# Kernel tuning notes

Hardware: AMD Instinct MI355X
Metric: run time of the kernel (lower is better)

Reference implementation:

```python
import jax, jax.numpy as jnp
import numpy as np

EPS = 1e-5


def _bn(v, gamma, beta, mean, var):
    # v: [n, c, L, 1]; per-channel eval-mode batchnorm
    scale = gamma / jnp.sqrt(var + EPS)
    return v * scale[None, :, None, None] + (beta - mean * scale)[None, :, None, None]


def _conv1x1(v, w, b):
    # v: [n, c, L, 1], w: [o, c], b: [o] -> [n, o, L, 1]
    y = jnp.einsum('ncl,oc->nol', v[..., 0], w) + b[None, :, None]
    return y[..., None]


def setup_inputs() -> dict:
    key = jax.random.key(0)
    ks = jax.random.split(key, 16)
    N, C, H, W, MIP = 8, 256, 112, 112, 8
    return {
        'x': jax.random.normal(ks[0], (N, C, H, W), dtype=jnp.float32),
        'bn1_gamma': jax.random.uniform(ks[1], (C,), dtype=jnp.float32),
        'bn1_beta': jax.random.normal(ks[2], (C,), dtype=jnp.float32) * 0.1,
        'bn1_mean': jax.random.normal(ks[3], (C,), dtype=jnp.float32) * 0.1,
        'bn1_var': jax.random.uniform(ks[4], (C,), dtype=jnp.float32) + 0.5,
        'bn2_gamma': jax.random.uniform(ks[5], (C,), dtype=jnp.float32),
        'bn2_beta': jax.random.normal(ks[6], (C,), dtype=jnp.float32) * 0.1,
        'bn2_mean': jax.random.normal(ks[7], (C,), dtype=jnp.float32) * 0.1,
        'bn2_var': jax.random.uniform(ks[8], (C,), dtype=jnp.float32) + 0.5,
        'ds_w': jax.random.normal(ks[9], (MIP, C), dtype=jnp.float32) * (1.0 / np.sqrt(C)),
        'ds_b': jax.random.normal(ks[10], (MIP,), dtype=jnp.float32) * 0.01,
        'us_w': jax.random.normal(ks[11], (C, MIP), dtype=jnp.float32) * (1.0 / np.sqrt(MIP)),
        'us_b': jax.random.normal(ks[12], (C,), dtype=jnp.float32) * 0.01,
    }


def reference(x, bn1_gamma, bn1_beta, bn1_mean, bn1_var,
              bn2_gamma, bn2_beta, bn2_mean, bn2_var,
              ds_w, ds_b, us_w, us_b):
    identity = x
    # dual-axis average pooling
    x_h = jnp.mean(x, axis=3, keepdims=True)                 # [n, c, h, 1]
    x_w = jnp.mean(x, axis=2, keepdims=True).transpose(0, 1, 3, 2)  # [n, c, w, 1]
    # batchnorm (eval mode)
    x_h = _bn(x_h, bn1_gamma, bn1_beta, bn1_mean, bn1_var)
    x_w = _bn(x_w, bn2_gamma, bn2_beta, bn2_mean, bn2_var)
    # channel-reduce 1x1 conv + relu
    d_h = jax.nn.relu(_conv1x1(x_h, ds_w, ds_b))             # [n, mip, h, 1]
    d_w = jax.nn.relu(_conv1x1(x_w, ds_w, ds_b))             # [n, mip, w, 1]
    # channel-expand 1x1 conv + sigmoid
    a_h = jax.nn.sigmoid(_conv1x1(d_h, us_w, us_b))          # [n, c, h, 1]
    a_w = jax.nn.sigmoid(_conv1x1(d_w, us_w, us_b))          # [n, c, w, 1]
    a_w = a_w.transpose(0, 1, 3, 2)                          # [n, c, 1, w]
    out = identity * a_w * a_h + identity
    # h_swish: x * relu6(x + 3) / 6
    return out * jnp.clip(out + 3.0, 0.0, 6.0) * (1.0 / 6.0)
```

## Files before the change

kernel.cpp:

```cpp
#include <hip/hip_runtime.h>
#include <math.h>

#define NN 8
#define CC 256
#define HH 112
#define WW 112
#define MIP 8
#define EPS 1e-5f

typedef float nvec4 __attribute__((ext_vector_type(4)));


__global__ __launch_bounds__(256) void pool_kernel(const float* __restrict__ x,
                                                   float* __restrict__ pool) {
    __shared__ float rowpart[HH][29];
    __shared__ float4 colpart[8][28];
    const int b = blockIdx.x;
    const int n = b / CC;
    const int c = b % CC;
    const int t = threadIdx.x;

    const nvec4* p4 = (const nvec4*)(x + (size_t)b * (HH * WW));

    if (t < 224) {
        const int g = t / 28;
        const int j = t % 28;
        float4 ca = make_float4(0.f, 0.f, 0.f, 0.f);
#pragma unroll
        for (int k = 0; k < 14; ++k) {
            const int r = g + 8 * k;
            nvec4 v = __builtin_nontemporal_load(&p4[r * 28 + j]);
            ca.x += v.x; ca.y += v.y; ca.z += v.z; ca.w += v.w;
            rowpart[r][j] = v.x + v.y + v.z + v.w;
        }
        colpart[g][j] = ca;
    }
    __syncthreads();

    if (t < HH) {
        float s = 0.f;
#pragma unroll
        for (int j = 0; j < 28; ++j) s += rowpart[t][j];
        pool[((size_t)(n * HH + t)) * CC + c] = s * (1.0f / WW);
    } else if (t < 112 + WW) {
        const int w = t - 112;
        const float* cp = (const float*)&colpart[0][0];
        float s = 0.f;
#pragma unroll
        for (int g = 0; g < 8; ++g) s += cp[g * 112 + w];
        pool[(size_t)(NN * HH * CC) + ((size_t)(n * WW + w)) * CC + c] = s * (1.0f / HH);
    }
}

__global__ __launch_bounds__(256) void att_kernel(
    float* __restrict__ pool,
    const float* __restrict__ bn1_g, const float* __restrict__ bn1_b,
    const float* __restrict__ bn1_m, const float* __restrict__ bn1_v,
    const float* __restrict__ bn2_g, const float* __restrict__ bn2_b,
    const float* __restrict__ bn2_m, const float* __restrict__ bn2_v,
    const float* __restrict__ ds_w, const float* __restrict__ ds_b,
    const float* __restrict__ us_w, const float* __restrict__ us_b) {
    __shared__ float s[CC];
    __shared__ float dsh[MIP];

    const int branch = blockIdx.y;
    const int c = threadIdx.x;

    const float* g  = branch ? bn2_g : bn1_g;
    const float* be = branch ? bn2_b : bn1_b;
    const float* mn = branch ? bn2_m : bn1_m;
    const float* vr = branch ? bn2_v : bn1_v;

    const size_t idx = (size_t)branch * (NN * HH * CC) + (size_t)blockIdx.x * CC + c;

    float v = pool[idx];
    float scale = g[c] * rsqrtf(vr[c] + EPS);
    float vb = v * scale + (be[c] - mn[c] * scale);
    s[c] = vb;
    __syncthreads();

    {
        const int grp = c >> 5;
        const int l = c & 31;
        float partial = 0.f;
#pragma unroll
        for (int k = 0; k < CC / 32; ++k) {
            const int cc = l + k * 32;
            partial += ds_w[grp * CC + cc] * s[cc];
        }
#pragma unroll
        for (int off = 16; off > 0; off >>= 1)
            partial += __shfl_down(partial, off, 32);
        if (l == 0) dsh[grp] = fmaxf(partial + ds_b[grp], 0.f);
    }
    __syncthreads();

    float acc = us_b[c];
#pragma unroll
    for (int m = 0; m < MIP; ++m) acc += us_w[c * MIP + m] * dsh[m];
    pool[idx] = 1.0f / (1.0f + expf(-acc));
}

__global__ __launch_bounds__(256) void apply_kernel(const float* __restrict__ x,
                                                    const float* __restrict__ att,
                                                    float* __restrict__ out) {
    __shared__ float ah[HH];
    __shared__ float aw[WW];
    const int b = blockIdx.x;
    const int n = b / CC;
    const int c = b % CC;
    const int tid = threadIdx.x;

    if (tid < HH) {
        ah[tid] = att[((size_t)(n * HH + tid)) * CC + c];
    } else if (tid >= 128 && tid < 128 + WW) {
        const int w = tid - 128;
        aw[w] = att[(size_t)(NN * HH * CC) + ((size_t)(n * WW + w)) * CC + c];
    }
    __syncthreads();

    const nvec4* xp = (const nvec4*)(x + (size_t)b * (HH * WW));
    nvec4* op = (nvec4*)(out + (size_t)b * (HH * WW));
#pragma unroll 4
    for (int i = tid; i < HH * (WW / 4); i += 256) {
        const int h = i / (WW / 4);
        const int w4 = i % (WW / 4);
        nvec4 xv = __builtin_nontemporal_load(&xp[i]);
        const float a_h = ah[h];
        nvec4 o;
        o.x = xv.x * (aw[w4 * 4 + 0] * a_h) + xv.x;
        o.y = xv.y * (aw[w4 * 4 + 1] * a_h) + xv.y;
        o.z = xv.z * (aw[w4 * 4 + 2] * a_h) + xv.z;
        o.w = xv.w * (aw[w4 * 4 + 3] * a_h) + xv.w;
        nvec4 r;
        r.x = o.x * fminf(fmaxf(o.x + 3.0f, 0.0f), 6.0f) * (1.0f / 6.0f);
        r.y = o.y * fminf(fmaxf(o.y + 3.0f, 0.0f), 6.0f) * (1.0f / 6.0f);
        r.z = o.z * fminf(fmaxf(o.z + 3.0f, 0.0f), 6.0f) * (1.0f / 6.0f);
        r.w = o.w * fminf(fmaxf(o.w + 3.0f, 0.0f), 6.0f) * (1.0f / 6.0f);
        __builtin_nontemporal_store(r, &op[i]);
    }
}

extern "C" void kernel_launch(void* const* d_in, const int* in_sizes, int n_in,
                              void* d_out, int out_size, void* d_ws, size_t ws_size,
                              hipStream_t stream) {
    const float* x     = (const float*)d_in[0];
    const float* bn1_g = (const float*)d_in[1];
    const float* bn1_b = (const float*)d_in[2];
    const float* bn1_m = (const float*)d_in[3];
    const float* bn1_v = (const float*)d_in[4];
    const float* bn2_g = (const float*)d_in[5];
    const float* bn2_b = (const float*)d_in[6];
    const float* bn2_m = (const float*)d_in[7];
    const float* bn2_v = (const float*)d_in[8];
    const float* ds_w  = (const float*)d_in[9];
    const float* ds_b  = (const float*)d_in[10];
    const float* us_w  = (const float*)d_in[11];
    const float* us_b  = (const float*)d_in[12];
    float* out = (float*)d_out;
    float* pool = (float*)d_ws;

    pool_kernel<<<NN * CC, 256, 0, stream>>>(x, pool);
    att_kernel<<<dim3(NN * HH, 2), 256, 0, stream>>>(pool,
        bn1_g, bn1_b, bn1_m, bn1_v, bn2_g, bn2_b, bn2_m, bn2_v,
        ds_w, ds_b, us_w, us_b);
    apply_kernel<<<NN * CC, 256, 0, stream>>>(x, pool, out);
}
```

Measured before the change: 223.1 us.

## Fuse pool, attention and apply into one persistent kernel with grid barriers

Replaces three kernel launches with a single persistent kernel of 512 blocks that loops over work items and separates the pooling, attention and apply phases with a software grid barrier built on atomics. The aim is to remove launch gaps and tail effects between the three stages. In exchange it relies on all 512 blocks being resident at once, since the spin barrier (with a timeout break) is unsafe otherwise. It also uses fewer blocks per phase, which may reduce memory-level parallelism for the bandwidth-bound pooling and apply passes.

```diff
diff --git a/kernel.cpp b/kernel.cpp
--- a/kernel.cpp
+++ b/kernel.cpp
@@ -7,137 +7,181 @@
 #define WW 112
 #define MIP 8
 #define EPS 1e-5f
+#define NBLK 512
+#define NREP 4
+#define NPOS (NN * HH)
 
 typedef float nvec4 __attribute__((ext_vector_type(4)));
 
-
-__global__ __launch_bounds__(256) void pool_kernel(const float* __restrict__ x,
-                                                   float* __restrict__ pool) {
-    __shared__ float rowpart[HH][29];
-    __shared__ float4 colpart[8][28];
-    const int b = blockIdx.x;
-    const int n = b / CC;
-    const int c = b % CC;
-    const int t = threadIdx.x;
-
-    const nvec4* p4 = (const nvec4*)(x + (size_t)b * (HH * WW));
-
-    if (t < 224) {
-        const int g = t / 28;
-        const int j = t % 28;
-        float4 ca = make_float4(0.f, 0.f, 0.f, 0.f);
-#pragma unroll
-        for (int k = 0; k < 14; ++k) {
-            const int r = g + 8 * k;
-            nvec4 v = __builtin_nontemporal_load(&p4[r * 28 + j]);
-            ca.x += v.x; ca.y += v.y; ca.z += v.z; ca.w += v.w;
-            rowpart[r][j] = v.x + v.y + v.z + v.w;
-        }
-        colpart[g][j] = ca;
-    }
+__device__ int g_cnt = 0;
+__device__ int g_gen = 0;
+
+__device__ __forceinline__ void grid_barrier() {
     __syncthreads();
-
-    if (t < HH) {
-        float s = 0.f;
-#pragma unroll
-        for (int j = 0; j < 28; ++j) s += rowpart[t][j];
-        pool[((size_t)(n * HH + t)) * CC + c] = s * (1.0f / WW);
-    } else if (t < 112 + WW) {
-        const int w = t - 112;
-        const float* cp = (const float*)&colpart[0][0];
-        float s = 0.f;
-#pragma unroll
-        for (int g = 0; g < 8; ++g) s += cp[g * 112 + w];
-        pool[(size_t)(NN * HH * CC) + ((size_t)(n * WW + w)) * CC + c] = s * (1.0f / HH);
-    }
+    if (threadIdx.x == 0) {
+        __threadfence();
+        const int my_gen = __hip_atomic_load(&g_gen, __ATOMIC_ACQUIRE,
+                                             __HIP_MEMORY_SCOPE_AGENT);
+        const int prev = __hip_atomic_fetch_add(&g_cnt, 1, __ATOMIC_ACQ_REL,
+                                                __HIP_MEMORY_SCOPE_AGENT);
+        if (prev == NBLK - 1) {
+            __hip_atomic_store(&g_cnt, 0, __ATOMIC_RELAXED,
+                               __HIP_MEMORY_SCOPE_AGENT);
+            __hip_atomic_fetch_add(&g_gen, 1, __ATOMIC_RELEASE,
+                                   __HIP_MEMORY_SCOPE_AGENT);
+        } else {
+            int spins = 0;
+            while (__hip_atomic_load(&g_gen, __ATOMIC_ACQUIRE,
+                                     __HIP_MEMORY_SCOPE_AGENT) == my_gen) {
+                __builtin_amdgcn_s_sleep(2);
+                if (++spins > (1 << 22)) break;
+            }
+        }
+        __threadfence();
+    }
+    __syncthreads();
 }
 
-__global__ __launch_bounds__(256) void att_kernel(
-    float* __restrict__ pool,
+__global__ __launch_bounds__(256, 4) void fused_kernel(
+    const float* __restrict__ x,
     const float* __restrict__ bn1_g, const float* __restrict__ bn1_b,
     const float* __restrict__ bn1_m, const float* __restrict__ bn1_v,
     const float* __restrict__ bn2_g, const float* __restrict__ bn2_b,
     const float* __restrict__ bn2_m, const float* __restrict__ bn2_v,
     const float* __restrict__ ds_w, const float* __restrict__ ds_b,
-    const float* __restrict__ us_w, const float* __restrict__ us_b) {
-    __shared__ float s[CC];
-    __shared__ float dsh[MIP];
-
-    const int branch = blockIdx.y;
-    const int c = threadIdx.x;
-
-    const float* g  = branch ? bn2_g : bn1_g;
-    const float* be = branch ? bn2_b : bn1_b;
-    const float* mn = branch ? bn2_m : bn1_m;
-    const float* vr = branch ? bn2_v : bn1_v;
-
-    const size_t idx = (size_t)branch * (NN * HH * CC) + (size_t)blockIdx.x * CC + c;
-
-    float v = pool[idx];
-    float scale = g[c] * rsqrtf(vr[c] + EPS);
-    float vb = v * scale + (be[c] - mn[c] * scale);
-    s[c] = vb;
-    __syncthreads();
-
-    {
-        const int grp = c >> 5;
-        const int l = c & 31;
-        float partial = 0.f;
-#pragma unroll
-        for (int k = 0; k < CC / 32; ++k) {
-            const int cc = l + k * 32;
-            partial += ds_w[grp * CC + cc] * s[cc];
-        }
-#pragma unroll
-        for (int off = 16; off > 0; off >>= 1)
-            partial += __shfl_down(partial, off, 32);
-        if (l == 0) dsh[grp] = fmaxf(partial + ds_b[grp], 0.f);
-    }
-    __syncthreads();
-
-    float acc = us_b[c];
-#pragma unroll
-    for (int m = 0; m < MIP; ++m) acc += us_w[c * MIP + m] * dsh[m];
-    pool[idx] = 1.0f / (1.0f + expf(-acc));
-}
-
-__global__ __launch_bounds__(256) void apply_kernel(const float* __restrict__ x,
-                                                    const float* __restrict__ att,
-                                                    float* __restrict__ out) {
-    __shared__ float ah[HH];
-    __shared__ float aw[WW];
-    const int b = blockIdx.x;
-    const int n = b / CC;
-    const int c = b % CC;
-    const int tid = threadIdx.x;
-
-    if (tid < HH) {
-        ah[tid] = att[((size_t)(n * HH + tid)) * CC + c];
-    } else if (tid >= 128 && tid < 128 + WW) {
-        const int w = tid - 128;
-        aw[w] = att[(size_t)(NN * HH * CC) + ((size_t)(n * WW + w)) * CC + c];
-    }
-    __syncthreads();
-
-    const nvec4* xp = (const nvec4*)(x + (size_t)b * (HH * WW));
-    nvec4* op = (nvec4*)(out + (size_t)b * (HH * WW));
+    const float* __restrict__ us_w, const float* __restrict__ us_b,
+    float* __restrict__ pool, float* __restrict__ out) {
+    const int t = threadIdx.x;
+
+    __shared__ union {
+        struct { float rowpart[HH][29]; float4 colpart[8][28]; } p1;
+        struct { float s[CC]; float dsh[MIP]; } p2;
+        struct { float ah[HH]; float aw[WW]; } p3;
+    } sm;
+
+#pragma unroll 1
+    for (int rep = 0; rep < NREP; ++rep) {
+        const int b = blockIdx.x + rep * NBLK;
+        const int n = b / CC;
+        const int c = b % CC;
+        const nvec4* p4 = (const nvec4*)(x + (size_t)b * (HH * WW));
+
+        if (t < 224) {
+            const int g = t / 28;
+            const int j = t % 28;
+            float4 ca = make_float4(0.f, 0.f, 0.f, 0.f);
+#pragma unroll
+            for (int k = 0; k < 14; ++k) {
+                const int r = g + 8 * k;
+                nvec4 v = __builtin_nontemporal_load(&p4[r * 28 + j]);
+                ca.x += v.x; ca.y += v.y; ca.z += v.z; ca.w += v.w;
+                sm.p1.rowpart[r][j] = v.x + v.y + v.z + v.w;
+            }
+            sm.p1.colpart[g][j] = ca;
+        }
+        __syncthreads();
+
+        if (t < HH) {
+            float s = 0.f;
+#pragma unroll
+            for (int j = 0; j < 28; ++j) s += sm.p1.rowpart[t][j];
+            pool[((size_t)(n * HH + t)) * CC + c] = s * (1.0f / WW);
+        } else if (t < 112 + WW) {
+            const int w = t - 112;
+            const float* cp = (const float*)&sm.p1.colpart[0][0];
+            float s = 0.f;
+#pragma unroll
+            for (int g = 0; g < 8; ++g) s += cp[g * 112 + w];
+            pool[(size_t)(NN * HH * CC) + ((size_t)(n * WW + w)) * CC + c] =
+                s * (1.0f / HH);
+        }
+        __syncthreads();
+    }
+    grid_barrier();
+
+#pragma unroll 1
+    for (int rep = 0; rep < NREP; ++rep) {
+        const int item = blockIdx.x + rep * NBLK;
+        const bool active = item < 2 * NPOS;
+        const int it = active ? item : 0;
+        const int branch = it >= NPOS;
+        const int pos = it - branch * NPOS;
+        const int c = t;
+
+        const float* g  = branch ? bn2_g : bn1_g;
+        const float* be = branch ? bn2_b : bn1_b;
+        const float* mn = branch ? bn2_m : bn1_m;
+        const float* vr = branch ? bn2_v : bn1_v;
+
+        const size_t idx =
+            (size_t)branch * (NN * HH * CC) + (size_t)pos * CC + c;
+
+        const float v = pool[idx];
+        const float scale = g[c] * rsqrtf(vr[c] + EPS);
+        const float vb = v * scale + (be[c] - mn[c] * scale);
+        sm.p2.s[c] = vb;
+        __syncthreads();
+
+        {
+            const int grp = c >> 5;
+            const int l = c & 31;
+            float partial = 0.f;
+#pragma unroll
+            for (int k = 0; k < CC / 32; ++k) {
+                const int cc = l + k * 32;
+                partial += ds_w[grp * CC + cc] * sm.p2.s[cc];
+            }
+#pragma unroll
+            for (int off = 16; off > 0; off >>= 1)
+                partial += __shfl_down(partial, off, 32);
+            if (l == 0) sm.p2.dsh[grp] = fmaxf(partial + ds_b[grp], 0.f);
+        }
+        __syncthreads();
+
+        float acc = us_b[c];
+#pragma unroll
+        for (int m = 0; m < MIP; ++m) acc += us_w[c * MIP + m] * sm.p2.dsh[m];
+        if (active) pool[idx] = 1.0f / (1.0f + expf(-acc));
+        __syncthreads();
+    }
+    grid_barrier();
+
+#pragma unroll 1
+    for (int rep = 0; rep < NREP; ++rep) {
+        const int b = blockIdx.x + rep * NBLK;
+        const int n = b / CC;
+        const int c = b % CC;
+
+        if (t < HH) {
+            sm.p3.ah[t] = pool[((size_t)(n * HH + t)) * CC + c];
+        } else if (t >= 128 && t < 128 + WW) {
+            const int w = t - 128;
+            sm.p3.aw[w] =
+                pool[(size_t)(NN * HH * CC) + ((size_t)(n * WW + w)) * CC + c];
+        }
+        __syncthreads();
+
+        const nvec4* xp = (const nvec4*)(x + (size_t)b * (HH * WW));
+        nvec4* op = (nvec4*)(out + (size_t)b * (HH * WW));
 #pragma unroll 4
-    for (int i = tid; i < HH * (WW / 4); i += 256) {
-        const int h = i / (WW / 4);
-        const int w4 = i % (WW / 4);
-        nvec4 xv = __builtin_nontemporal_load(&xp[i]);
-        const float a_h = ah[h];
-        nvec4 o;
-        o.x = xv.x * (aw[w4 * 4 + 0] * a_h) + xv.x;
-        o.y = xv.y * (aw[w4 * 4 + 1] * a_h) + xv.y;
-        o.z = xv.z * (aw[w4 * 4 + 2] * a_h) + xv.z;
-        o.w = xv.w * (aw[w4 * 4 + 3] * a_h) + xv.w;
-        nvec4 r;
-        r.x = o.x * fminf(fmaxf(o.x + 3.0f, 0.0f), 6.0f) * (1.0f / 6.0f);
-        r.y = o.y * fminf(fmaxf(o.y + 3.0f, 0.0f), 6.0f) * (1.0f / 6.0f);
-        r.z = o.z * fminf(fmaxf(o.z + 3.0f, 0.0f), 6.0f) * (1.0f / 6.0f);
-        r.w = o.w * fminf(fmaxf(o.w + 3.0f, 0.0f), 6.0f) * (1.0f / 6.0f);
-        __builtin_nontemporal_store(r, &op[i]);
+        for (int i = t; i < HH * (WW / 4); i += 256) {
+            const int h = i / (WW / 4);
+            const int w4 = i % (WW / 4);
+            nvec4 xv = __builtin_nontemporal_load(&xp[i]);
+            const float a_h = sm.p3.ah[h];
+            nvec4 o;
+            o.x = xv.x * (sm.p3.aw[w4 * 4 + 0] * a_h) + xv.x;
+            o.y = xv.y * (sm.p3.aw[w4 * 4 + 1] * a_h) + xv.y;
+            o.z = xv.z * (sm.p3.aw[w4 * 4 + 2] * a_h) + xv.z;
+            o.w = xv.w * (sm.p3.aw[w4 * 4 + 3] * a_h) + xv.w;
+            nvec4 r;
+            r.x = o.x * fminf(fmaxf(o.x + 3.0f, 0.0f), 6.0f) * (1.0f / 6.0f);
+            r.y = o.y * fminf(fmaxf(o.y + 3.0f, 0.0f), 6.0f) * (1.0f / 6.0f);
+            r.z = o.z * fminf(fmaxf(o.z + 3.0f, 0.0f), 6.0f) * (1.0f / 6.0f);
+            r.w = o.w * fminf(fmaxf(o.w + 3.0f, 0.0f), 6.0f) * (1.0f / 6.0f);
+            __builtin_nontemporal_store(r, &op[i]);
+        }
+        __syncthreads();
     }
 }
 
@@ -157,12 +201,10 @@
     const float* ds_b  = (const float*)d_in[10];
     const float* us_w  = (const float*)d_in[11];
     const float* us_b  = (const float*)d_in[12];
-    float* out = (float*)d_out;
+    float* out  = (float*)d_out;
     float* pool = (float*)d_ws;
 
-    pool_kernel<<<NN * CC, 256, 0, stream>>>(x, pool);
-    att_kernel<<<dim3(NN * HH, 2), 256, 0, stream>>>(pool,
+    fused_kernel<<<NBLK, 256, 0, stream>>>(x,
         bn1_g, bn1_b, bn1_m, bn1_v, bn2_g, bn2_b, bn2_m, bn2_v,
-        ds_w, ds_b, us_w, us_b);
-    apply_kernel<<<NN * CC, 256, 0, stream>>>(x, pool, out);
+        ds_w, ds_b, us_w, us_b, pool, out);
 }
```

Result: slower. 388.1 us (+73.9%).

## Fuse BN into pooling and fold attention MLP into apply kernel

Applied to the files above, without the earlier changes.

Batchnorm is now applied inside the pooling kernel, and the separate attention kernel is removed. Each apply block handles two channels and recomputes the down-projection, ReLU, up-projection and sigmoid for all 224 positions of its image using wave shuffles. This cuts a launch and a global round-trip of the attention map. In exchange, the small MLP is computed redundantly 128 times per image, and the grid is halved to 1024 blocks, each streaming two planes.

```diff
diff --git a/kernel.cpp b/kernel.cpp
--- a/kernel.cpp
+++ b/kernel.cpp
@@ -7,12 +7,18 @@
 #define WW 112
 #define MIP 8
 #define EPS 1e-5f
+#define NPOS 224
+#define WOFF (NN * HH * CC)
 
 typedef float nvec4 __attribute__((ext_vector_type(4)));
 
-
-__global__ __launch_bounds__(256) void pool_kernel(const float* __restrict__ x,
-                                                   float* __restrict__ pool) {
+__global__ __launch_bounds__(256) void pool_bn_kernel(
+    const float* __restrict__ x,
+    const float* __restrict__ bn1_g, const float* __restrict__ bn1_b,
+    const float* __restrict__ bn1_m, const float* __restrict__ bn1_v,
+    const float* __restrict__ bn2_g, const float* __restrict__ bn2_b,
+    const float* __restrict__ bn2_m, const float* __restrict__ bn2_v,
+    float* __restrict__ pool) {
     __shared__ float rowpart[HH][29];
     __shared__ float4 colpart[8][28];
     const int b = blockIdx.x;
@@ -41,103 +47,124 @@
         float s = 0.f;
 #pragma unroll
         for (int j = 0; j < 28; ++j) s += rowpart[t][j];
-        pool[((size_t)(n * HH + t)) * CC + c] = s * (1.0f / WW);
+        const float sc = bn1_g[c] * rsqrtf(bn1_v[c] + EPS);
+        const float sh = bn1_b[c] - bn1_m[c] * sc;
+        pool[((size_t)(n * HH + t)) * CC + c] = (s * (1.0f / WW)) * sc + sh;
     } else if (t < 112 + WW) {
         const int w = t - 112;
         const float* cp = (const float*)&colpart[0][0];
         float s = 0.f;
 #pragma unroll
         for (int g = 0; g < 8; ++g) s += cp[g * 112 + w];
-        pool[(size_t)(NN * HH * CC) + ((size_t)(n * WW + w)) * CC + c] = s * (1.0f / HH);
+        const float sc = bn2_g[c] * rsqrtf(bn2_v[c] + EPS);
+        const float sh = bn2_b[c] - bn2_m[c] * sc;
+        pool[(size_t)WOFF + ((size_t)(n * WW + w)) * CC + c] =
+            (s * (1.0f / HH)) * sc + sh;
     }
 }
 
-__global__ __launch_bounds__(256) void att_kernel(
-    float* __restrict__ pool,
-    const float* __restrict__ bn1_g, const float* __restrict__ bn1_b,
-    const float* __restrict__ bn1_m, const float* __restrict__ bn1_v,
-    const float* __restrict__ bn2_g, const float* __restrict__ bn2_b,
-    const float* __restrict__ bn2_m, const float* __restrict__ bn2_v,
+__global__ __launch_bounds__(256) void att_apply_kernel(
+    const float* __restrict__ x,
     const float* __restrict__ ds_w, const float* __restrict__ ds_b,
-    const float* __restrict__ us_w, const float* __restrict__ us_b) {
-    __shared__ float s[CC];
-    __shared__ float dsh[MIP];
+    const float* __restrict__ us_w, const float* __restrict__ us_b,
+    const float* __restrict__ pool, float* __restrict__ out) {
+    __shared__ float aL[2][NPOS];
 
-    const int branch = blockIdx.y;
-    const int c = threadIdx.x;
+    const int b = blockIdx.x;
+    const int n = b >> 7;
+    const int c0 = (b & 127) << 1;
+    const int t = threadIdx.x;
+    const int l = t & 63;
+    const int wave = t >> 6;
+    const int m = l & 7;
 
-    const float* g  = branch ? bn2_g : bn1_g;
-    const float* be = branch ? bn2_b : bn1_b;
-    const float* mn = branch ? bn2_m : bn1_m;
-    const float* vr = branch ? bn2_v : bn1_v;
+    const nvec4* dsw4 = (const nvec4*)ds_w;
+    nvec4 w4[8];
+#pragma unroll
+    for (int mm = 0; mm < 8; ++mm) w4[mm] = dsw4[mm * 64 + l];
+    const float dsb  = ds_b[m];
+    const float usw0 = us_w[c0 * MIP + m];
+    const float usw1 = us_w[(c0 + 1) * MIP + m];
+    const float usb0 = us_b[c0];
+    const float usb1 = us_b[c0 + 1];
 
-    const size_t idx = (size_t)branch * (NN * HH * CC) + (size_t)blockIdx.x * CC + c;
+    const float* poolH = pool + (size_t)(n * HH) * CC;
+    const float* poolW = pool + WOFF + (size_t)(n * WW) * CC;
 
-    float v = pool[idx];
-    float scale = g[c] * rsqrtf(vr[c] + EPS);
-    float vb = v * scale + (be[c] - mn[c] * scale);
-    s[c] = vb;
-    __syncthreads();
+    const bool b0 = (l & 1) != 0, b1 = (l & 2) != 0, b2 = (l & 4) != 0;
 
-    {
-        const int grp = c >> 5;
-        const int l = c & 31;
-        float partial = 0.f;
+#pragma unroll 1
+    for (int i = 0; i < 56; ++i) {
+        const int p = wave * 56 + i;
+        const float* row = (p < HH) ? (poolH + (size_t)p * CC)
+                                    : (poolW + (size_t)(p - HH) * CC);
+        nvec4 v = ((const nvec4*)row)[l];
+        float r[8];
 #pragma unroll
-        for (int k = 0; k < CC / 32; ++k) {
-            const int cc = l + k * 32;
-            partial += ds_w[grp * CC + cc] * s[cc];
+        for (int mm = 0; mm < 8; ++mm)
+            r[mm] = v.x * w4[mm].x + v.y * w4[mm].y +
+                    v.z * w4[mm].z + v.w * w4[mm].w;
+
+        float s_[4];
+#pragma unroll
+        for (int q = 0; q < 4; ++q) {
+            float snd = b0 ? r[2 * q] : r[2 * q + 1];
+            float kp  = b0 ? r[2 * q + 1] : r[2 * q];
+            s_[q] = kp + __shfl_xor(snd, 1);
         }
+        float u_[2];
 #pragma unroll
-        for (int off = 16; off > 0; off >>= 1)
-            partial += __shfl_down(partial, off, 32);
-        if (l == 0) dsh[grp] = fmaxf(partial + ds_b[grp], 0.f);
+        for (int q = 0; q < 2; ++q) {
+            float snd = b1 ? s_[2 * q] : s_[2 * q + 1];
+            float kp  = b1 ? s_[2 * q + 1] : s_[2 * q];
+            u_[q] = kp + __shfl_xor(snd, 2);
+        }
+        float d;
+        {
+            float snd = b2 ? u_[0] : u_[1];
+            float kp  = b2 ? u_[1] : u_[0];
+            d = kp + __shfl_xor(snd, 4);
+        }
+        d += __shfl_xor(d, 8);
+        d += __shfl_xor(d, 16);
+        d += __shfl_xor(d, 32);
+        const float dsh = fmaxf(d + dsb, 0.f);
+
+        float p0 = usw0 * dsh, p1 = usw1 * dsh;
+        p0 += __shfl_xor(p0, 1); p0 += __shfl_xor(p0, 2); p0 += __shfl_xor(p0, 4);
+        p1 += __shfl_xor(p1, 1); p1 += __shfl_xor(p1, 2); p1 += __shfl_xor(p1, 4);
+        if (l == 0) {
+            aL[0][p] = 1.0f / (1.0f + expf(-(usb0 + p0)));
+            aL[1][p] = 1.0f / (1.0f + expf(-(usb1 + p1)));
+        }
     }
     __syncthreads();
 
-    float acc = us_b[c];
-#pragma unroll
-    for (int m = 0; m < MIP; ++m) acc += us_w[c * MIP + m] * dsh[m];
-    pool[idx] = 1.0f / (1.0f + expf(-acc));
-}
-
-__global__ __launch_bounds__(256) void apply_kernel(const float* __restrict__ x,
-                                                    const float* __restrict__ att,
-                                                    float* __restrict__ out) {
-    __shared__ float ah[HH];
-    __shared__ float aw[WW];
-    const int b = blockIdx.x;
-    const int n = b / CC;
-    const int c = b % CC;
-    const int tid = threadIdx.x;
-
-    if (tid < HH) {
-        ah[tid] = att[((size_t)(n * HH + tid)) * CC + c];
-    } else if (tid >= 128 && tid < 128 + WW) {
-        const int w = tid - 128;
-        aw[w] = att[(size_t)(NN * HH * CC) + ((size_t)(n * WW + w)) * CC + c];
-    }
-    __syncthreads();
-
-    const nvec4* xp = (const nvec4*)(x + (size_t)b * (HH * WW));
-    nvec4* op = (nvec4*)(out + (size_t)b * (HH * WW));
+#pragma unroll 1
+    for (int ci = 0; ci < 2; ++ci) {
+        const size_t plane = (size_t)(n * CC + c0 + ci) * (HH * WW);
+        const nvec4* xp = (const nvec4*)(x + plane);
+        nvec4* op = (nvec4*)(out + plane);
+        const float* ah = aL[ci];
+        const float* aw = aL[ci] + HH;
 #pragma unroll 4
-    for (int i = tid; i < HH * (WW / 4); i += 256) {
-        const int h = i / (WW / 4);
-        const int w4 = i % (WW / 4);
-        nvec4 xv = __builtin_nontemporal_load(&xp[i]);
-        const float a_h = ah[h];
-        nvec4 o;
-        o.x = xv.x * (aw[w4 * 4 + 0] * a_h) + xv.x;
-        o.y = xv.y * (aw[w4 * 4 + 1] * a_h) + xv.y;
-        o.z = xv.z * (aw[w4 * 4 + 2] * a_h) + xv.z;
-        o.w = xv.w * (aw[w4 * 4 + 3] * a_h) + xv.w;
-        nvec4 r;
-        r.x = o.x * fminf(fmaxf(o.x + 3.0f, 0.0f), 6.0f) * (1.0f / 6.0f);
-        r.y = o.y * fminf(fmaxf(o.y + 3.0f, 0.0f), 6.0f) * (1.0f / 6.0f);
-        r.z = o.z * fminf(fmaxf(o.z + 3.0f, 0.0f), 6.0f) * (1.0f / 6.0f);
-        r.w = o.w * fminf(fmaxf(o.w + 3.0f, 0.0f), 6.0f) * (1.0f / 6.0f);
-        __builtin_nontemporal_store(r, &op[i]);
+        for (int i = t; i < HH * (WW / 4); i += 256) {
+            const int h = i / (WW / 4);
+            const int w4i = i % (WW / 4);
+            nvec4 xv = __builtin_nontemporal_load(&xp[i]);
+            const float a_h = ah[h];
+            nvec4 o;
+            o.x = xv.x * (aw[w4i * 4 + 0] * a_h) + xv.x;
+            o.y = xv.y * (aw[w4i * 4 + 1] * a_h) + xv.y;
+            o.z = xv.z * (aw[w4i * 4 + 2] * a_h) + xv.z;
+            o.w = xv.w * (aw[w4i * 4 + 3] * a_h) + xv.w;
+            nvec4 rr;
+            rr.x = o.x * fminf(fmaxf(o.x + 3.0f, 0.0f), 6.0f) * (1.0f / 6.0f);
+            rr.y = o.y * fminf(fmaxf(o.y + 3.0f, 0.0f), 6.0f) * (1.0f / 6.0f);
+            rr.z = o.z * fminf(fmaxf(o.z + 3.0f, 0.0f), 6.0f) * (1.0f / 6.0f);
+            rr.w = o.w * fminf(fmaxf(o.w + 3.0f, 0.0f), 6.0f) * (1.0f / 6.0f);
+            __builtin_nontemporal_store(rr, &op[i]);
+        }
     }
 }
 
@@ -157,12 +184,11 @@
     const float* ds_b  = (const float*)d_in[10];
     const float* us_w  = (const float*)d_in[11];
     const float* us_b  = (const float*)d_in[12];
-    float* out = (float*)d_out;
+    float* out  = (float*)d_out;
     float* pool = (float*)d_ws;
 
-    pool_kernel<<<NN * CC, 256, 0, stream>>>(x, pool);
-    att_kernel<<<dim3(NN * HH, 2), 256, 0, stream>>>(pool,
-        bn1_g, bn1_b, bn1_m, bn1_v, bn2_g, bn2_b, bn2_m, bn2_v,
-        ds_w, ds_b, us_w, us_b);
-    apply_kernel<<<NN * CC, 256, 0, stream>>>(x, pool, out);
+    pool_bn_kernel<<<NN * CC, 256, 0, stream>>>(x,
+        bn1_g, bn1_b, bn1_m, bn1_v, bn2_g, bn2_b, bn2_m, bn2_v, pool);
+    att_apply_kernel<<<NN * (CC / 2), 256, 0, stream>>>(x,
+        ds_w, ds_b, us_w, us_b, pool, out);
 }
```

Measured after the change: 263.8 us. +18.2%, slower.
